# Kernel tuning notes

Hardware: AMD Instinct MI355X
Metric: run time of the kernel (lower is better)

## Reference

```python
import jax, jax.numpy as jnp
import numpy as np

B, N, S, D, H = 32, 16384, 8, 64, 128  # batch, num_inputs, num_slots, slot_size(==input_size), mlp_hidden
ITERS = 3
EPS = 1e-8
LN_EPS = 1e-5


def _ln(x, g, b):
    m = jnp.mean(x, axis=-1, keepdims=True)
    v = jnp.mean((x - m) ** 2, axis=-1, keepdims=True)
    return (x - m) * jax.lax.rsqrt(v + LN_EPS) * g + b


def setup_inputs() -> dict:
    key = jax.random.key(0)
    ks = jax.random.split(key, 20)
    s = 0.02
    return {
        "x": jax.random.normal(ks[0], (B, N, D), jnp.float32),
        "slot_noise": jax.random.normal(ks[1], (B, S, D), jnp.float32),
        "slots_mu": jax.random.normal(ks[2], (1, S, D), jnp.float32),
        "slots_log_sigma": jax.random.normal(ks[3], (1, S, D), jnp.float32) * 0.1,
        "ln_in_g": jnp.ones((D,), jnp.float32), "ln_in_b": jnp.zeros((D,), jnp.float32),
        "ln_slot_g": jnp.ones((D,), jnp.float32), "ln_slot_b": jnp.zeros((D,), jnp.float32),
        "ln_mlp_g": jnp.ones((D,), jnp.float32), "ln_mlp_b": jnp.zeros((D,), jnp.float32),
        "Wq": jax.random.normal(ks[4], (D, D), jnp.float32) * s,
        "Wk": jax.random.normal(ks[5], (D, D), jnp.float32) * s,
        "Wv": jax.random.normal(ks[6], (D, D), jnp.float32) * s,
        "W_ih": jax.random.normal(ks[7], (3 * D, D), jnp.float32) * s,
        "W_hh": jax.random.normal(ks[8], (3 * D, D), jnp.float32) * s,
        "b_ih": jnp.zeros((3 * D,), jnp.float32),
        "b_hh": jnp.zeros((3 * D,), jnp.float32),
        "W1": jax.random.normal(ks[9], (H, D), jnp.float32) * s,
        "b1": jnp.zeros((H,), jnp.float32),
        "W2": jax.random.normal(ks[10], (D, H), jnp.float32) * s,
        "b2": jnp.zeros((D,), jnp.float32),
    }


def reference(x, slot_noise, slots_mu, slots_log_sigma,
              ln_in_g, ln_in_b, ln_slot_g, ln_slot_b, ln_mlp_g, ln_mlp_b,
              Wq, Wk, Wv, W_ih, W_hh, b_ih, b_hh, W1, b1, W2, b2):
    inputs = _ln(x, ln_in_g, ln_in_b)                      # [B,N,D]
    keys = inputs @ Wk.T                                   # [B,N,D]
    values = inputs @ Wv.T                                 # [B,N,D]
    slots = slots_mu + jnp.exp(slots_log_sigma) * slot_noise  # [B,S,D]
    scale = D ** (-0.5)
    for _ in range(ITERS):
        slots_prev = slots
        q = (_ln(slots, ln_slot_g, ln_slot_b) @ Wq.T) * scale   # [B,S,D]
        attn = jax.nn.softmax(jnp.einsum('bnd,bsd->bns', keys, q), axis=2) + EPS
        attn = attn / jnp.sum(attn, axis=1, keepdims=True)      # weighted mean over inputs
        updates = jnp.einsum('bns,bnd->bsd', attn, values)      # [B,S,D]
        # GRUCell(update, hidden=slots_prev), torch semantics
        gi = updates @ W_ih.T + b_ih
        gh = slots_prev @ W_hh.T + b_hh
        i_r, i_z, i_n = jnp.split(gi, 3, axis=-1)
        h_r, h_z, h_n = jnp.split(gh, 3, axis=-1)
        r = jax.nn.sigmoid(i_r + h_r)
        z = jax.nn.sigmoid(i_z + h_z)
        n = jnp.tanh(i_n + r * h_n)
        upd = (1.0 - z) * n + z * slots_prev
        # residual MLP (full_skip=False: residual around updates)
        slots = upd + jax.nn.relu(_ln(upd, ln_mlp_g, ln_mlp_b) @ W1.T + b1) @ W2.T + b2
    return slots
```

## Files before the change

### kernel.cpp

```cpp
#include <hip/hip_runtime.h>

#define BB 32
#define NN 16384

typedef __attribute__((ext_vector_type(4))) float f4;
typedef __attribute__((ext_vector_type(8))) short short8;

__device__ __forceinline__ unsigned int f2bf(float f) {
  unsigned int u = __float_as_uint(f);
  return (u + 0x7fffu + ((u >> 16) & 1u)) >> 16;
}
__device__ __forceinline__ short bfs(float f) { return (short)f2bf(f); }

__global__ void __launch_bounds__(256) prep_kernel(
    const float* __restrict__ Wk, const float* __restrict__ Wv,
    unsigned short* __restrict__ Wkb, unsigned short* __restrict__ Wvb)
{
  int id = blockIdx.x * 256 + threadIdx.x;
  Wkb[id] = (unsigned short)f2bf(Wk[id]);
  Wvb[id] = (unsigned short)f2bf(Wv[id]);
}

__global__ void __launch_bounds__(64) init_q_kernel(
    const float* __restrict__ noise, const float* __restrict__ mu,
    const float* __restrict__ lsig, float* __restrict__ slots,
    const float* __restrict__ gs, const float* __restrict__ bsl,
    const float* __restrict__ Wq, unsigned short* __restrict__ qb)
{
  const int bsi = blockIdx.x, l = threadIdx.x;
  const int idx = bsi * 64 + l;
  __shared__ float sh[64];
  float v = mu[idx & 511] + __expf(lsig[idx & 511]) * noise[idx];
  slots[idx] = v;
  float sm = v, sq = v * v;
#pragma unroll
  for (int m = 1; m < 64; m <<= 1) { sm += __shfl_xor(sm, m); sq += __shfl_xor(sq, m); }
  float mean = sm * (1.f / 64.f);
  float var = sq * (1.f / 64.f) - mean * mean;
  sh[l] = (v - mean) * rsqrtf(var + 1e-5f) * gs[l] + bsl[l];
  float acc = 0.f;
  const float* w = Wq + l * 64;
  for (int k = 0; k < 64; ++k) acc += sh[k] * w[k];
  qb[idx] = (unsigned short)f2bf(acc * 0.125f);
}

__global__ void __launch_bounds__(256) proj_kernel(
    const float* __restrict__ x, const float* __restrict__ gin, const float* __restrict__ bin,
    const unsigned short* __restrict__ Wkb, const unsigned short* __restrict__ Wvb,
    unsigned short* __restrict__ Kf, unsigned short* __restrict__ Vtf)
{
  const int blk = blockIdx.x;
  const int tid = threadIdx.x, wave = tid >> 6, lane = tid & 63;
  const int l15 = lane & 15, quad = lane >> 4;
  const int b = blk >> 5;
  const size_t row0 = ((size_t)blk << 9) + (wave << 4) + l15;
  const float* xp = x + row0 * 64 + quad * 8;

  const int k0 = quad * 8;
  f4 g0a = *(const f4*)(gin + k0),      g0b = *(const f4*)(gin + k0 + 4);
  f4 g1a = *(const f4*)(gin + k0 + 32), g1b = *(const f4*)(gin + k0 + 36);
  f4 h0a = *(const f4*)(bin + k0),      h0b = *(const f4*)(bin + k0 + 4);
  f4 h1a = *(const f4*)(bin + k0 + 32), h1b = *(const f4*)(bin + k0 + 36);

  f4 c0 = *(const f4*)xp, c1 = *(const f4*)(xp + 4);
  f4 c2 = *(const f4*)(xp + 32), c3 = *(const f4*)(xp + 36);

  for (int g = 0; g < 8; ++g) {
    f4 p0, p1, p2, p3;
    if (g < 7) {
      const float* np = xp + (size_t)(g + 1) * 4096;
      p0 = *(const f4*)np;        p1 = *(const f4*)(np + 4);
      p2 = *(const f4*)(np + 32); p3 = *(const f4*)(np + 36);
    }
    float sm = 0.f, sq = 0.f;
#pragma unroll
    for (int j = 0; j < 4; ++j) {
      float v0 = c0[j], v1 = c1[j], v2 = c2[j], v3 = c3[j];
      sm += v0 + v1 + v2 + v3;
      sq += v0 * v0 + v1 * v1 + v2 * v2 + v3 * v3;
    }
    sm += __shfl_xor(sm, 16); sq += __shfl_xor(sq, 16);
    sm += __shfl_xor(sm, 32); sq += __shfl_xor(sq, 32);
    const float mean = sm * (1.f / 64.f);
    const float var = sq * (1.f / 64.f) - mean * mean;
    const float rstd = rsqrtf(var + 1e-5f);

    short8 a0, a1;
#pragma unroll
    for (int j = 0; j < 4; ++j) {
      a0[j]     = bfs((c0[j] - mean) * rstd * g0a[j] + h0a[j]);
      a0[j + 4] = bfs((c1[j] - mean) * rstd * g0b[j] + h0b[j]);
      a1[j]     = bfs((c2[j] - mean) * rstd * g1a[j] + h1a[j]);
      a1[j + 4] = bfs((c3[j] - mean) * rstd * g1b[j] + h1b[j]);
    }

    const int nblk = ((blk & 31) << 5) + (g << 2) + wave;
    unsigned short* kbase = Kf + (((size_t)b << 20) + (nblk << 10));
    unsigned short* vbase = Vtf + (((size_t)b << 20) + (nblk << 10));

#pragma unroll
    for (int dt = 0; dt < 4; ++dt) {
      const unsigned short* wkp = Wkb + ((dt << 4) + l15) * 64 + k0;
      const unsigned short* wvp = Wvb + ((dt << 4) + l15) * 64 + k0;
      short8 wk0 = *(const short8*)wkp, wk1 = *(const short8*)(wkp + 32);
      short8 wv0 = *(const short8*)wvp, wv1 = *(const short8*)(wvp + 32);
      f4 ak = {0.f, 0.f, 0.f, 0.f}, av = {0.f, 0.f, 0.f, 0.f};
      ak = __builtin_amdgcn_mfma_f32_16x16x32_bf16(wk0, a0, ak, 0, 0, 0);
      ak = __builtin_amdgcn_mfma_f32_16x16x32_bf16(wk1, a1, ak, 0, 0, 0);
      av = __builtin_amdgcn_mfma_f32_16x16x32_bf16(a0, wv0, av, 0, 0, 0);
      av = __builtin_amdgcn_mfma_f32_16x16x32_bf16(a1, wv1, av, 0, 0, 0);
      uint2 kk;
      kk.x = f2bf(ak[0]) | (f2bf(ak[1]) << 16);
      kk.y = f2bf(ak[2]) | (f2bf(ak[3]) << 16);
      *(uint2*)(kbase + (((dt << 1) + (quad >> 1)) << 7) + (l15 << 3) + ((quad & 1) << 2)) = kk;
      uint2 vv;
      vv.x = f2bf(av[0]) | (f2bf(av[1]) << 16);
      vv.y = f2bf(av[2]) | (f2bf(av[3]) << 16);
      *(uint2*)(vbase + (((dt << 4) + l15) << 4) + (quad << 2)) = vv;
    }
    c0 = p0; c1 = p1; c2 = p2; c3 = p3;
  }
}

__global__ void __launch_bounds__(256) reduce_kernel(
    const unsigned short* __restrict__ Kf, const unsigned short* __restrict__ Vtf,
    const unsigned short* __restrict__ qb,
    float* __restrict__ Wpart, float* __restrict__ cpart)
{
  __shared__ __align__(16) unsigned short Pt[4][16][40];
  __shared__ float red[4][512];
  __shared__ float cred[4][8];

  const int tid = threadIdx.x, wave = tid >> 6, lane = tid & 63;
  const int l15 = lane & 15, quad = lane >> 4;
  const int b = blockIdx.x >> 5, ch = blockIdx.x & 31;

  const unsigned short* qrow = qb + (((b << 3) + (l15 & 7)) << 6) + quad * 8;
  short8 qf0 = *(const short8*)qrow;
  short8 qf1 = *(const short8*)(qrow + 32);

  const unsigned short* Kb = Kf + ((size_t)b << 20);
  const unsigned short* Vb = Vtf + ((size_t)b << 20);

  f4 wacc[4];
#pragma unroll
  for (int t = 0; t < 4; ++t) wacc[t] = (f4){0.f, 0.f, 0.f, 0.f};
  float cacc = 0.f;
  const int nblk_base = (ch << 5) + (wave << 3);

  short8 ck[4], cv[4];
  {
    const unsigned short* ka = Kb + (nblk_base << 10) + (quad << 7) + (l15 << 3);
    ck[0] = *(const short8*)ka;
    ck[1] = *(const short8*)(ka + 512);
    ck[2] = *(const short8*)(ka + 1024);
    ck[3] = *(const short8*)(ka + 1536);
#pragma unroll
    for (int t = 0; t < 4; ++t)
      cv[t] = *(const short8*)(Vb + ((size_t)(nblk_base + (quad >> 1)) << 10) +
                               (((t << 4) + l15) << 4) + ((quad & 1) << 3));
  }

#pragma unroll
  for (int u = 0; u < 4; ++u) {
    short8 nk[4], nv[4];
    if (u < 3) {
      const int nblk = nblk_base + 2 * (u + 1);
      const unsigned short* ka = Kb + (nblk << 10) + (quad << 7) + (l15 << 3);
      nk[0] = *(const short8*)ka;
      nk[1] = *(const short8*)(ka + 512);
      nk[2] = *(const short8*)(ka + 1024);
      nk[3] = *(const short8*)(ka + 1536);
#pragma unroll
      for (int t = 0; t < 4; ++t)
        nv[t] = *(const short8*)(Vb + ((size_t)(nblk + (quad >> 1)) << 10) +
                                 (((t << 4) + l15) << 4) + ((quad & 1) << 3));
    }

#pragma unroll
    for (int h = 0; h < 2; ++h) {
      f4 lg = {0.f, 0.f, 0.f, 0.f};
      lg = __builtin_amdgcn_mfma_f32_16x16x32_bf16(ck[h * 2], qf0, lg, 0, 0, 0);
      lg = __builtin_amdgcn_mfma_f32_16x16x32_bf16(ck[h * 2 + 1], qf1, lg, 0, 0, 0);
      float p[4];
#pragma unroll
      for (int r2 = 0; r2 < 4; ++r2) {
        float e = __expf(lg[r2]);
        float ss = e;
        ss += __shfl_xor(ss, 1);
        ss += __shfl_xor(ss, 2);
        ss += __shfl_xor(ss, 4);
        p[r2] = e * __builtin_amdgcn_rcpf(ss);
        cacc += p[r2];
      }
      unsigned short* pw = &Pt[wave][l15][h * 16 + quad * 4];
      *(unsigned int*)pw = f2bf(p[0]) | (f2bf(p[1]) << 16);
      *(unsigned int*)(pw + 2) = f2bf(p[2]) | (f2bf(p[3]) << 16);
    }
    short8 pf = *(const short8*)&Pt[wave][l15][quad * 8];
#pragma unroll
    for (int t = 0; t < 4; ++t)
      wacc[t] = __builtin_amdgcn_mfma_f32_16x16x32_bf16(pf, cv[t], wacc[t], 0, 0, 0);

#pragma unroll
    for (int i = 0; i < 4; ++i) { ck[i] = nk[i]; cv[i] = nv[i]; }
  }

  cacc += __shfl_xor(cacc, 16);
  cacc += __shfl_xor(cacc, 32);
  if (lane < 8) cred[wave][lane] = cacc;
  if (quad < 2) {
#pragma unroll
    for (int t = 0; t < 4; ++t)
#pragma unroll
      for (int r2 = 0; r2 < 4; ++r2)
        red[wave][(quad * 4 + r2) * 64 + (t << 4) + l15] = wacc[t][r2];
  }
  __syncthreads();
  for (int i = tid; i < 512; i += 256)
    Wpart[(size_t)blockIdx.x * 512 + i] = red[0][i] + red[1][i] + red[2][i] + red[3][i];
  if (tid < 8)
    cpart[blockIdx.x * 8 + tid] = cred[0][tid] + cred[1][tid] + cred[2][tid] + cred[3][tid];
}

__global__ void __launch_bounds__(256) update_kernel(
    const float* __restrict__ Wpart, const float* __restrict__ cpart,
    const float* __restrict__ slots, float* __restrict__ out,
    const float* __restrict__ W_ih, const float* __restrict__ W_hh,
    const float* __restrict__ b_ih, const float* __restrict__ b_hh,
    const float* __restrict__ g_mlp, const float* __restrict__ b_mlp,
    const float* __restrict__ W1, const float* __restrict__ b1,
    const float* __restrict__ W2, const float* __restrict__ b2,
    const float* __restrict__ gs, const float* __restrict__ bsl,
    const float* __restrict__ Wq, unsigned short* __restrict__ qb, int make_q)
{
  const int bs = blockIdx.x;
  const int b = bs >> 3, s = bs & 7;
  const int tid = threadIdx.x;
  const int l = tid & 63, cq = tid >> 6;
  __shared__ float wred[4][64];
  __shared__ float credS[4];
  __shared__ float u_sh[64], sp_sh[64], giA[192], ghA[192], uln_sh[64], h_sh[128];

  float wp = 0.f, cp2 = 0.f;
  for (int c = cq * 8; c < cq * 8 + 8; ++c) {
    wp += Wpart[(size_t)(((b << 5) + c) * 8 + s) * 64 + l];
    cp2 += cpart[((b << 5) + c) * 8 + s];
  }
  wred[cq][l] = wp;
  if (l == 0) credS[cq] = cp2;
  __syncthreads();

  float sp = 0.f;
  if (tid < 64) {
    const float cs = credS[0] + credS[1] + credS[2] + credS[3];
    const float u = (wred[0][l] + wred[1][l] + wred[2][l] + wred[3][l]) / cs;
    sp = slots[(b * 8 + s) * 64 + l];
    u_sh[l] = u; sp_sh[l] = sp;
  }
  __syncthreads();

  if (tid < 192) {
    float accI = b_ih[tid], accH = b_hh[tid];
    const float* wi = W_ih + tid * 64;
    const float* wh = W_hh + tid * 64;
    for (int k = 0; k < 64; ++k) { accI += u_sh[k] * wi[k]; accH += sp_sh[k] * wh[k]; }
    giA[tid] = accI; ghA[tid] = accH;
  }
  __syncthreads();

  float upd = 0.f;
  if (tid < 64) {
    const float rg = 1.f / (1.f + __expf(-(giA[l] + ghA[l])));
    const float zg = 1.f / (1.f + __expf(-(giA[64 + l] + ghA[64 + l])));
    const float ng = tanhf(giA[128 + l] + rg * ghA[128 + l]);
    upd = (1.f - zg) * ng + zg * sp;
    float sm = upd, sq = upd * upd;
#pragma unroll
    for (int m = 1; m < 64; m <<= 1) { sm += __shfl_xor(sm, m); sq += __shfl_xor(sq, m); }
    const float mean = sm * (1.f / 64.f);
    const float var = sq * (1.f / 64.f) - mean * mean;
    uln_sh[l] = (upd - mean) * rsqrtf(var + 1e-5f) * g_mlp[l] + b_mlp[l];
  }
  __syncthreads();

  if (tid < 128) {
    float acc = b1[tid];
    const float* w1 = W1 + tid * 64;
    for (int k = 0; k < 64; ++k) acc += uln_sh[k] * w1[k];
    h_sh[tid] = fmaxf(acc, 0.f);
  }
  __syncthreads();

  if (tid < 64) {
    float acc = b2[l];
    const float* w2 = W2 + l * 128;
    for (int k = 0; k < 128; ++k) acc += h_sh[k] * w2[k];
    const float sv = upd + acc;
    out[(b * 8 + s) * 64 + l] = sv;
    if (make_q) {
      float sm2 = sv, sq2 = sv * sv;
#pragma unroll
      for (int m = 1; m < 64; m <<= 1) { sm2 += __shfl_xor(sm2, m); sq2 += __shfl_xor(sq2, m); }
      const float mean2 = sm2 * (1.f / 64.f);
      const float var2 = sq2 * (1.f / 64.f) - mean2 * mean2;
      u_sh[l] = (sv - mean2) * rsqrtf(var2 + 1e-5f) * gs[l] + bsl[l];
      float qa = 0.f;
      const float* w = Wq + l * 64;
      for (int k = 0; k < 64; ++k) qa += u_sh[k] * w[k];
      qb[(b * 8 + s) * 64 + l] = (unsigned short)f2bf(qa * 0.125f);
    }
  }
}

extern "C" void kernel_launch(void* const* d_in, const int* in_sizes, int n_in,
                              void* d_out, int out_size, void* d_ws, size_t ws_size,
                              hipStream_t stream) {
  const float* x       = (const float*)d_in[0];
  const float* noise   = (const float*)d_in[1];
  const float* mu      = (const float*)d_in[2];
  const float* lsig    = (const float*)d_in[3];
  const float* ln_in_g = (const float*)d_in[4];
  const float* ln_in_b = (const float*)d_in[5];
  const float* ln_sl_g = (const float*)d_in[6];
  const float* ln_sl_b = (const float*)d_in[7];
  const float* ln_ml_g = (const float*)d_in[8];
  const float* ln_ml_b = (const float*)d_in[9];
  const float* Wq      = (const float*)d_in[10];
  const float* Wk      = (const float*)d_in[11];
  const float* Wv      = (const float*)d_in[12];
  const float* W_ih    = (const float*)d_in[13];
  const float* W_hh    = (const float*)d_in[14];
  const float* b_ih    = (const float*)d_in[15];
  const float* b_hh    = (const float*)d_in[16];
  const float* W1      = (const float*)d_in[17];
  const float* b1      = (const float*)d_in[18];
  const float* W2      = (const float*)d_in[19];
  const float* b2      = (const float*)d_in[20];

  unsigned short* Kw  = (unsigned short*)d_ws;
  unsigned short* Vt  = Kw + (size_t)BB * NN * 64;
  unsigned short* Wkb = Vt + (size_t)BB * NN * 64;
  unsigned short* Wvb = Wkb + 4096;
  unsigned short* qb  = Wvb + 4096;
  float* slots = (float*)(qb + 16384);
  float* Wpart = slots + 32 * 8 * 64;
  float* cpart = Wpart + (size_t)1024 * 512;

  prep_kernel<<<dim3(16), dim3(256), 0, stream>>>(Wk, Wv, Wkb, Wvb);
  init_q_kernel<<<dim3(256), dim3(64), 0, stream>>>(
      noise, mu, lsig, slots, ln_sl_g, ln_sl_b, Wq, qb);
  proj_kernel<<<dim3(1024), dim3(256), 0, stream>>>(
      x, ln_in_g, ln_in_b, Wkb, Wvb, Kw, Vt);

  for (int it = 0; it < 3; ++it) {
    reduce_kernel<<<dim3(1024), dim3(256), 0, stream>>>(Kw, Vt, qb, Wpart, cpart);
    update_kernel<<<dim3(256), dim3(256), 0, stream>>>(
        Wpart, cpart, slots, (it == 2) ? (float*)d_out : slots,
        W_ih, W_hh, b_ih, b_hh, ln_ml_g, ln_ml_b, W1, b1, W2, b2,
        ln_sl_g, ln_sl_b, Wq, qb, (it < 2) ? 1 : 0);
  }
}
```

Before: 344.5 us.

## Fold Wk and Wv into query and GRU weights, attend directly on normalized inputs

Drops the separate K and V projections. Query logits are computed as LN(x)·(Wq^T Wk applied to slot LN), and the value projection is folded into the GRU input weights (W_ih·Wv), precomputed in prep_kernel. The first attention pass fuses input layernorm and writes bf16 normalized x once. Later iterations reread that buffer, transposing it through LDS to form the weighted sum. This halves the stored and reread per-iteration data (one bf16 tensor instead of K and V) and removes the projection MFMAs, at the cost of LDS transpose work and slightly different rounding.

```diff
diff --git a/kernel.cpp b/kernel.cpp
--- a/kernel.cpp
+++ b/kernel.cpp
@@ -13,19 +13,29 @@
 __device__ __forceinline__ short bfs(float f) { return (short)f2bf(f); }
 
 __global__ void __launch_bounds__(256) prep_kernel(
-    const float* __restrict__ Wk, const float* __restrict__ Wv,
-    unsigned short* __restrict__ Wkb, unsigned short* __restrict__ Wvb)
+    const float* __restrict__ Wq, const float* __restrict__ Wk,
+    const float* __restrict__ W_ih, const float* __restrict__ Wv,
+    float* __restrict__ M, float* __restrict__ Wihv)
 {
   int id = blockIdx.x * 256 + threadIdx.x;
-  Wkb[id] = (unsigned short)f2bf(Wk[id]);
-  Wvb[id] = (unsigned short)f2bf(Wv[id]);
-}
-
-__global__ void __launch_bounds__(64) init_q_kernel(
+  if (id < 4096) {
+    int e1 = id >> 6, e2 = id & 63;
+    float acc = 0.f;
+    for (int d = 0; d < 64; ++d) acc += Wq[d * 64 + e1] * Wk[d * 64 + e2];
+    M[id] = acc;
+  } else {
+    int t = (id - 4096) >> 6, e = id & 63;
+    float acc = 0.f;
+    for (int k = 0; k < 64; ++k) acc += W_ih[t * 64 + k] * Wv[k * 64 + e];
+    Wihv[t * 64 + e] = acc;
+  }
+}
+
+__global__ void __launch_bounds__(64) init_qk_kernel(
     const float* __restrict__ noise, const float* __restrict__ mu,
     const float* __restrict__ lsig, float* __restrict__ slots,
     const float* __restrict__ gs, const float* __restrict__ bsl,
-    const float* __restrict__ Wq, unsigned short* __restrict__ qb)
+    const float* __restrict__ M, unsigned short* __restrict__ qkb)
 {
   const int bsi = blockIdx.x, l = threadIdx.x;
   const int idx = bsi * 64 + l;
@@ -39,171 +49,170 @@
   float var = sq * (1.f / 64.f) - mean * mean;
   sh[l] = (v - mean) * rsqrtf(var + 1e-5f) * gs[l] + bsl[l];
   float acc = 0.f;
-  const float* w = Wq + l * 64;
-  for (int k = 0; k < 64; ++k) acc += sh[k] * w[k];
-  qb[idx] = (unsigned short)f2bf(acc * 0.125f);
-}
-
-__global__ void __launch_bounds__(256) proj_kernel(
-    const float* __restrict__ x, const float* __restrict__ gin, const float* __restrict__ bin,
-    const unsigned short* __restrict__ Wkb, const unsigned short* __restrict__ Wvb,
-    unsigned short* __restrict__ Kf, unsigned short* __restrict__ Vtf)
-{
-  const int blk = blockIdx.x;
-  const int tid = threadIdx.x, wave = tid >> 6, lane = tid & 63;
-  const int l15 = lane & 15, quad = lane >> 4;
-  const int b = blk >> 5;
-  const size_t row0 = ((size_t)blk << 9) + (wave << 4) + l15;
-  const float* xp = x + row0 * 64 + quad * 8;
-
-  const int k0 = quad * 8;
-  f4 g0a = *(const f4*)(gin + k0),      g0b = *(const f4*)(gin + k0 + 4);
-  f4 g1a = *(const f4*)(gin + k0 + 32), g1b = *(const f4*)(gin + k0 + 36);
-  f4 h0a = *(const f4*)(bin + k0),      h0b = *(const f4*)(bin + k0 + 4);
-  f4 h1a = *(const f4*)(bin + k0 + 32), h1b = *(const f4*)(bin + k0 + 36);
-
-  f4 c0 = *(const f4*)xp, c1 = *(const f4*)(xp + 4);
-  f4 c2 = *(const f4*)(xp + 32), c3 = *(const f4*)(xp + 36);
-
-  for (int g = 0; g < 8; ++g) {
-    f4 p0, p1, p2, p3;
-    if (g < 7) {
-      const float* np = xp + (size_t)(g + 1) * 4096;
-      p0 = *(const f4*)np;        p1 = *(const f4*)(np + 4);
-      p2 = *(const f4*)(np + 32); p3 = *(const f4*)(np + 36);
-    }
-    float sm = 0.f, sq = 0.f;
-#pragma unroll
-    for (int j = 0; j < 4; ++j) {
-      float v0 = c0[j], v1 = c1[j], v2 = c2[j], v3 = c3[j];
-      sm += v0 + v1 + v2 + v3;
-      sq += v0 * v0 + v1 * v1 + v2 * v2 + v3 * v3;
-    }
-    sm += __shfl_xor(sm, 16); sq += __shfl_xor(sq, 16);
-    sm += __shfl_xor(sm, 32); sq += __shfl_xor(sq, 32);
-    const float mean = sm * (1.f / 64.f);
-    const float var = sq * (1.f / 64.f) - mean * mean;
-    const float rstd = rsqrtf(var + 1e-5f);
-
-    short8 a0, a1;
-#pragma unroll
-    for (int j = 0; j < 4; ++j) {
-      a0[j]     = bfs((c0[j] - mean) * rstd * g0a[j] + h0a[j]);
-      a0[j + 4] = bfs((c1[j] - mean) * rstd * g0b[j] + h0b[j]);
-      a1[j]     = bfs((c2[j] - mean) * rstd * g1a[j] + h1a[j]);
-      a1[j + 4] = bfs((c3[j] - mean) * rstd * g1b[j] + h1b[j]);
-    }
-
-    const int nblk = ((blk & 31) << 5) + (g << 2) + wave;
-    unsigned short* kbase = Kf + (((size_t)b << 20) + (nblk << 10));
-    unsigned short* vbase = Vtf + (((size_t)b << 20) + (nblk << 10));
-
-#pragma unroll
-    for (int dt = 0; dt < 4; ++dt) {
-      const unsigned short* wkp = Wkb + ((dt << 4) + l15) * 64 + k0;
-      const unsigned short* wvp = Wvb + ((dt << 4) + l15) * 64 + k0;
-      short8 wk0 = *(const short8*)wkp, wk1 = *(const short8*)(wkp + 32);
-      short8 wv0 = *(const short8*)wvp, wv1 = *(const short8*)(wvp + 32);
-      f4 ak = {0.f, 0.f, 0.f, 0.f}, av = {0.f, 0.f, 0.f, 0.f};
-      ak = __builtin_amdgcn_mfma_f32_16x16x32_bf16(wk0, a0, ak, 0, 0, 0);
-      ak = __builtin_amdgcn_mfma_f32_16x16x32_bf16(wk1, a1, ak, 0, 0, 0);
-      av = __builtin_amdgcn_mfma_f32_16x16x32_bf16(a0, wv0, av, 0, 0, 0);
-      av = __builtin_amdgcn_mfma_f32_16x16x32_bf16(a1, wv1, av, 0, 0, 0);
-      uint2 kk;
-      kk.x = f2bf(ak[0]) | (f2bf(ak[1]) << 16);
-      kk.y = f2bf(ak[2]) | (f2bf(ak[3]) << 16);
-      *(uint2*)(kbase + (((dt << 1) + (quad >> 1)) << 7) + (l15 << 3) + ((quad & 1) << 2)) = kk;
-      uint2 vv;
-      vv.x = f2bf(av[0]) | (f2bf(av[1]) << 16);
-      vv.y = f2bf(av[2]) | (f2bf(av[3]) << 16);
-      *(uint2*)(vbase + (((dt << 4) + l15) << 4) + (quad << 2)) = vv;
-    }
-    c0 = p0; c1 = p1; c2 = p2; c3 = p3;
-  }
-}
-
-__global__ void __launch_bounds__(256) reduce_kernel(
-    const unsigned short* __restrict__ Kf, const unsigned short* __restrict__ Vtf,
-    const unsigned short* __restrict__ qb,
+  for (int k = 0; k < 64; ++k) acc += sh[k] * M[k * 64 + l];
+  qkb[idx] = (unsigned short)f2bf(acc * 0.125f);
+}
+
+template <int MODE>
+__global__ void __launch_bounds__(256) attn_kernel(
+    const float* __restrict__ x, const unsigned short* __restrict__ Xin,
+    const float* __restrict__ gin, const float* __restrict__ bin,
+    unsigned short* __restrict__ Xout,
+    const unsigned short* __restrict__ qkb,
     float* __restrict__ Wpart, float* __restrict__ cpart)
 {
+  __shared__ __align__(16) unsigned short XT[4][4608];
   __shared__ __align__(16) unsigned short Pt[4][16][40];
   __shared__ float red[4][512];
   __shared__ float cred[4][8];
 
   const int tid = threadIdx.x, wave = tid >> 6, lane = tid & 63;
   const int l15 = lane & 15, quad = lane >> 4;
-  const int b = blockIdx.x >> 5, ch = blockIdx.x & 31;
-
-  const unsigned short* qrow = qb + (((b << 3) + (l15 & 7)) << 6) + quad * 8;
-  short8 qf0 = *(const short8*)qrow;
-  short8 qf1 = *(const short8*)(qrow + 32);
-
-  const unsigned short* Kb = Kf + ((size_t)b << 20);
-  const unsigned short* Vb = Vtf + ((size_t)b << 20);
+  const int blk = blockIdx.x;
+  const int b = blk >> 5;
+  const int k0 = quad * 8;
+
+  const unsigned short* qrow = qkb + (((b << 3) + (l15 & 7)) << 6) + k0;
+  const short8 qkA0 = *(const short8*)qrow;
+  const short8 qkA1 = *(const short8*)(qrow + 32);
+
+  f4 g0a, g0b, g1a, g1b, h0a, h0b, h1a, h1b;
+  if constexpr (MODE == 0) {
+    g0a = *(const f4*)(gin + k0);      g0b = *(const f4*)(gin + k0 + 4);
+    g1a = *(const f4*)(gin + k0 + 32); g1b = *(const f4*)(gin + k0 + 36);
+    h0a = *(const f4*)(bin + k0);      h0b = *(const f4*)(bin + k0 + 4);
+    h1a = *(const f4*)(bin + k0 + 32); h1b = *(const f4*)(bin + k0 + 36);
+  }
+
+  const size_t row00 = (size_t)blk * 512 + wave * 32 + l15;
+  unsigned short* xt = &XT[wave][0];
 
   f4 wacc[4];
 #pragma unroll
   for (int t = 0; t < 4; ++t) wacc[t] = (f4){0.f, 0.f, 0.f, 0.f};
   float cacc = 0.f;
-  const int nblk_base = (ch << 5) + (wave << 3);
-
-  short8 ck[4], cv[4];
-  {
-    const unsigned short* ka = Kb + (nblk_base << 10) + (quad << 7) + (l15 << 3);
-    ck[0] = *(const short8*)ka;
-    ck[1] = *(const short8*)(ka + 512);
-    ck[2] = *(const short8*)(ka + 1024);
-    ck[3] = *(const short8*)(ka + 1536);
-#pragma unroll
-    for (int t = 0; t < 4; ++t)
-      cv[t] = *(const short8*)(Vb + ((size_t)(nblk_base + (quad >> 1)) << 10) +
-                               (((t << 4) + l15) << 4) + ((quad & 1) << 3));
+
+  f4 cc[2][4];
+  short8 aa[2][2];
+  if constexpr (MODE == 0) {
+    const float* xp = x + row00 * 64 + k0;
+#pragma unroll
+    for (int s = 0; s < 2; ++s) {
+      const float* sp = xp + s * 1024;
+      cc[s][0] = *(const f4*)sp;        cc[s][1] = *(const f4*)(sp + 4);
+      cc[s][2] = *(const f4*)(sp + 32); cc[s][3] = *(const f4*)(sp + 36);
+    }
+  } else {
+    const unsigned short* xb = Xin + row00 * 64 + k0;
+#pragma unroll
+    for (int s = 0; s < 2; ++s) {
+      aa[s][0] = *(const short8*)(xb + s * 1024);
+      aa[s][1] = *(const short8*)(xb + s * 1024 + 32);
+    }
   }
 
 #pragma unroll
   for (int u = 0; u < 4; ++u) {
-    short8 nk[4], nv[4];
+    f4 nc[2][4];
+    short8 na[2][2];
     if (u < 3) {
-      const int nblk = nblk_base + 2 * (u + 1);
-      const unsigned short* ka = Kb + (nblk << 10) + (quad << 7) + (l15 << 3);
-      nk[0] = *(const short8*)ka;
-      nk[1] = *(const short8*)(ka + 512);
-      nk[2] = *(const short8*)(ka + 1024);
-      nk[3] = *(const short8*)(ka + 1536);
-#pragma unroll
-      for (int t = 0; t < 4; ++t)
-        nv[t] = *(const short8*)(Vb + ((size_t)(nblk + (quad >> 1)) << 10) +
-                                 (((t << 4) + l15) << 4) + ((quad & 1) << 3));
-    }
-
-#pragma unroll
-    for (int h = 0; h < 2; ++h) {
-      f4 lg = {0.f, 0.f, 0.f, 0.f};
-      lg = __builtin_amdgcn_mfma_f32_16x16x32_bf16(ck[h * 2], qf0, lg, 0, 0, 0);
-      lg = __builtin_amdgcn_mfma_f32_16x16x32_bf16(ck[h * 2 + 1], qf1, lg, 0, 0, 0);
+      if constexpr (MODE == 0) {
+        const float* xp = x + (row00 + (size_t)(u + 1) * 128) * 64 + k0;
+#pragma unroll
+        for (int s = 0; s < 2; ++s) {
+          const float* sp = xp + s * 1024;
+          nc[s][0] = *(const f4*)sp;        nc[s][1] = *(const f4*)(sp + 4);
+          nc[s][2] = *(const f4*)(sp + 32); nc[s][3] = *(const f4*)(sp + 36);
+        }
+      } else {
+        const unsigned short* xb = Xin + (row00 + (size_t)(u + 1) * 128) * 64 + k0;
+#pragma unroll
+        for (int s = 0; s < 2; ++s) {
+          na[s][0] = *(const short8*)(xb + s * 1024);
+          na[s][1] = *(const short8*)(xb + s * 1024 + 32);
+        }
+      }
+    }
+
+#pragma unroll
+    for (int s = 0; s < 2; ++s) {
+      short8 a0, a1;
+      if constexpr (MODE == 0) {
+        float sm = 0.f, sq = 0.f;
+#pragma unroll
+        for (int j = 0; j < 4; ++j) {
+          float v0 = cc[s][0][j], v1 = cc[s][1][j], v2 = cc[s][2][j], v3 = cc[s][3][j];
+          sm += v0 + v1 + v2 + v3;
+          sq += v0 * v0 + v1 * v1 + v2 * v2 + v3 * v3;
+        }
+        sm += __shfl_xor(sm, 16); sq += __shfl_xor(sq, 16);
+        sm += __shfl_xor(sm, 32); sq += __shfl_xor(sq, 32);
+        const float mean = sm * (1.f / 64.f);
+        const float var = sq * (1.f / 64.f) - mean * mean;
+        const float rstd = rsqrtf(var + 1e-5f);
+#pragma unroll
+        for (int j = 0; j < 4; ++j) {
+          a0[j]     = bfs((cc[s][0][j] - mean) * rstd * g0a[j] + h0a[j]);
+          a0[j + 4] = bfs((cc[s][1][j] - mean) * rstd * g0b[j] + h0b[j]);
+          a1[j]     = bfs((cc[s][2][j] - mean) * rstd * g1a[j] + h1a[j]);
+          a1[j + 4] = bfs((cc[s][3][j] - mean) * rstd * g1b[j] + h1b[j]);
+        }
+        unsigned short* xo = Xout + (row00 + (size_t)u * 128 + s * 16) * 64 + k0;
+        *(short8*)xo = a0;
+        *(short8*)(xo + 32) = a1;
+      } else {
+        a0 = aa[s][0]; a1 = aa[s][1];
+      }
+
+      {
+        const int nn = s * 16 + l15;
+        unsigned short* xb0 = xt + (quad << 3) + nn;
+#pragma unroll
+        for (int jj = 0; jj < 8; ++jj) {
+          xb0[(k0 + jj) * 72]        = (unsigned short)a0[jj];
+          xb0[(k0 + jj + 32) * 72]   = (unsigned short)a1[jj];
+        }
+      }
+
+      f4 lg = (f4){0.f, 0.f, 0.f, 0.f};
+      lg = __builtin_amdgcn_mfma_f32_16x16x32_bf16(a0, qkA0, lg, 0, 0, 0);
+      lg = __builtin_amdgcn_mfma_f32_16x16x32_bf16(a1, qkA1, lg, 0, 0, 0);
       float p[4];
 #pragma unroll
-      for (int r2 = 0; r2 < 4; ++r2) {
-        float e = __expf(lg[r2]);
+      for (int r = 0; r < 4; ++r) {
+        float e = __expf(lg[r]);
         float ss = e;
         ss += __shfl_xor(ss, 1);
         ss += __shfl_xor(ss, 2);
         ss += __shfl_xor(ss, 4);
-        p[r2] = e * __builtin_amdgcn_rcpf(ss);
-        cacc += p[r2];
-      }
-      unsigned short* pw = &Pt[wave][l15][h * 16 + quad * 4];
+        p[r] = e * __builtin_amdgcn_rcpf(ss);
+        cacc += p[r];
+      }
+      unsigned short* pw = &Pt[wave][l15][s * 16 + quad * 4];
       *(unsigned int*)pw = f2bf(p[0]) | (f2bf(p[1]) << 16);
       *(unsigned int*)(pw + 2) = f2bf(p[2]) | (f2bf(p[3]) << 16);
     }
+
     short8 pf = *(const short8*)&Pt[wave][l15][quad * 8];
 #pragma unroll
-    for (int t = 0; t < 4; ++t)
-      wacc[t] = __builtin_amdgcn_mfma_f32_16x16x32_bf16(pf, cv[t], wacc[t], 0, 0, 0);
-
-#pragma unroll
-    for (int i = 0; i < 4; ++i) { ck[i] = nk[i]; cv[i] = nv[i]; }
+    for (int t = 0; t < 4; ++t) {
+      const int rr = t * 16 + l15;
+      const short8 cvv =
+          *(const short8*)&xt[rr * 72 + (((rr >> 3) & 3) << 3) + (quad << 3)];
+      wacc[t] = __builtin_amdgcn_mfma_f32_16x16x32_bf16(pf, cvv, wacc[t], 0, 0, 0);
+    }
+
+    if (u < 3) {
+      if constexpr (MODE == 0) {
+#pragma unroll
+        for (int s = 0; s < 2; ++s)
+#pragma unroll
+          for (int j = 0; j < 4; ++j) cc[s][j] = nc[s][j];
+      } else {
+#pragma unroll
+        for (int s = 0; s < 2; ++s) { aa[s][0] = na[s][0]; aa[s][1] = na[s][1]; }
+      }
+    }
   }
 
   cacc += __shfl_xor(cacc, 16);
@@ -213,26 +222,26 @@
 #pragma unroll
     for (int t = 0; t < 4; ++t)
 #pragma unroll
-      for (int r2 = 0; r2 < 4; ++r2)
-        red[wave][(quad * 4 + r2) * 64 + (t << 4) + l15] = wacc[t][r2];
+      for (int r = 0; r < 4; ++r)
+        red[wave][(quad * 4 + r) * 64 + (t << 4) + l15] = wacc[t][r];
   }
   __syncthreads();
   for (int i = tid; i < 512; i += 256)
-    Wpart[(size_t)blockIdx.x * 512 + i] = red[0][i] + red[1][i] + red[2][i] + red[3][i];
+    Wpart[(size_t)blk * 512 + i] = red[0][i] + red[1][i] + red[2][i] + red[3][i];
   if (tid < 8)
-    cpart[blockIdx.x * 8 + tid] = cred[0][tid] + cred[1][tid] + cred[2][tid] + cred[3][tid];
+    cpart[blk * 8 + tid] = cred[0][tid] + cred[1][tid] + cred[2][tid] + cred[3][tid];
 }
 
 __global__ void __launch_bounds__(256) update_kernel(
     const float* __restrict__ Wpart, const float* __restrict__ cpart,
     const float* __restrict__ slots, float* __restrict__ out,
-    const float* __restrict__ W_ih, const float* __restrict__ W_hh,
+    const float* __restrict__ Wihv, const float* __restrict__ W_hh,
     const float* __restrict__ b_ih, const float* __restrict__ b_hh,
     const float* __restrict__ g_mlp, const float* __restrict__ b_mlp,
     const float* __restrict__ W1, const float* __restrict__ b1,
     const float* __restrict__ W2, const float* __restrict__ b2,
     const float* __restrict__ gs, const float* __restrict__ bsl,
-    const float* __restrict__ Wq, unsigned short* __restrict__ qb, int make_q)
+    const float* __restrict__ M, unsigned short* __restrict__ qkb, int make_q)
 {
   const int bs = blockIdx.x;
   const int b = bs >> 3, s = bs & 7;
@@ -262,7 +271,7 @@
 
   if (tid < 192) {
     float accI = b_ih[tid], accH = b_hh[tid];
-    const float* wi = W_ih + tid * 64;
+    const float* wi = Wihv + tid * 64;
     const float* wh = W_hh + tid * 64;
     for (int k = 0; k < 64; ++k) { accI += u_sh[k] * wi[k]; accH += sp_sh[k] * wh[k]; }
     giA[tid] = accI; ghA[tid] = accH;
@@ -306,9 +315,8 @@
       const float var2 = sq2 * (1.f / 64.f) - mean2 * mean2;
       u_sh[l] = (sv - mean2) * rsqrtf(var2 + 1e-5f) * gs[l] + bsl[l];
       float qa = 0.f;
-      const float* w = Wq + l * 64;
-      for (int k = 0; k < 64; ++k) qa += u_sh[k] * w[k];
-      qb[(b * 8 + s) * 64 + l] = (unsigned short)f2bf(qa * 0.125f);
+      for (int k = 0; k < 64; ++k) qa += u_sh[k] * M[k * 64 + l];
+      qkb[(b * 8 + s) * 64 + l] = (unsigned short)f2bf(qa * 0.125f);
     }
   }
 }
@@ -338,26 +346,28 @@
   const float* W2      = (const float*)d_in[19];
   const float* b2      = (const float*)d_in[20];
 
-  unsigned short* Kw  = (unsigned short*)d_ws;
-  unsigned short* Vt  = Kw + (size_t)BB * NN * 64;
-  unsigned short* Wkb = Vt + (size_t)BB * NN * 64;
-  unsigned short* Wvb = Wkb + 4096;
-  unsigned short* qb  = Wvb + 4096;
-  float* slots = (float*)(qb + 16384);
-  float* Wpart = slots + 32 * 8 * 64;
+  unsigned short* Xn  = (unsigned short*)d_ws;
+  unsigned short* qkb = Xn + (size_t)BB * NN * 64;
+  float* M     = (float*)(qkb + 16384);
+  float* Wihv  = M + 4096;
+  float* slots = Wihv + 12288;
+  float* Wpart = slots + 16384;
   float* cpart = Wpart + (size_t)1024 * 512;
 
-  prep_kernel<<<dim3(16), dim3(256), 0, stream>>>(Wk, Wv, Wkb, Wvb);
-  init_q_kernel<<<dim3(256), dim3(64), 0, stream>>>(
-      noise, mu, lsig, slots, ln_sl_g, ln_sl_b, Wq, qb);
-  proj_kernel<<<dim3(1024), dim3(256), 0, stream>>>(
-      x, ln_in_g, ln_in_b, Wkb, Wvb, Kw, Vt);
+  prep_kernel<<<dim3(64), dim3(256), 0, stream>>>(Wq, Wk, W_ih, Wv, M, Wihv);
+  init_qk_kernel<<<dim3(256), dim3(64), 0, stream>>>(
+      noise, mu, lsig, slots, ln_sl_g, ln_sl_b, M, qkb);
+
+  attn_kernel<0><<<dim3(1024), dim3(256), 0, stream>>>(
+      x, nullptr, ln_in_g, ln_in_b, Xn, qkb, Wpart, cpart);
 
   for (int it = 0; it < 3; ++it) {
-    reduce_kernel<<<dim3(1024), dim3(256), 0, stream>>>(Kw, Vt, qb, Wpart, cpart);
     update_kernel<<<dim3(256), dim3(256), 0, stream>>>(
         Wpart, cpart, slots, (it == 2) ? (float*)d_out : slots,
-        W_ih, W_hh, b_ih, b_hh, ln_ml_g, ln_ml_b, W1, b1, W2, b2,
-        ln_sl_g, ln_sl_b, Wq, qb, (it < 2) ? 1 : 0);
-  }
-}
+        Wihv, W_hh, b_ih, b_hh, ln_ml_g, ln_ml_b, W1, b1, W2, b2,
+        ln_sl_g, ln_sl_b, M, qkb, (it < 2) ? 1 : 0);
+    if (it < 2)
+      attn_kernel<1><<<dim3(1024), dim3(256), 0, stream>>>(
+          x, Xn, ln_in_g, ln_in_b, nullptr, qkb, Wpart, cpart);
+  }
+}
```

New measurement: 308.3 us. 1.12x faster.
